# Optimization experiments

Hardware: AMD Instinct MI355X
Metric: run time of the kernel (lower is better)

## Reference

```python
import jax, jax.numpy as jnp
import numpy as np

EPS = 1e-12  # F.normalize default eps


def setup_inputs() -> dict:
    key = jax.random.key(0)
    k1, k2, k3 = jax.random.split(key, 3)
    B, C, H, W = 4, 64, 64, 64
    background = jax.random.normal(k1, (B, C, H, W), dtype=jnp.float32)
    foreground = jax.random.normal(k2, (B, C, H, W), dtype=jnp.float32)
    # binary mask, broadcast over channels
    mask = jnp.round(jax.random.uniform(k3, (B, 1, H, W), dtype=jnp.float32))
    return {"background": background, "foreground": foreground, "mask": mask}


def _l2norm(x, axis):
    # matches torch F.normalize: x / max(||x||, eps)
    n = jnp.sqrt(jnp.sum(x * x, axis=axis, keepdims=True))
    return x / jnp.maximum(n, EPS)


def reference(background, foreground, mask):
    B, C, H, W = background.shape
    bg_flat = background.reshape(B, C, H * W)   # [B, C, K]
    fg_flat = foreground.reshape(B, C, H * W)   # [B, C, Q]
    norm_bg = _l2norm(bg_flat, axis=1)
    norm_fg = _l2norm(fg_flat, axis=1)
    # cosine-similarity scores [B, K, Q]
    attention = jnp.einsum('bck,bcq->bkq', norm_bg, norm_fg)
    attention = jax.nn.softmax(attention, axis=1)  # over bg (key) axis
    attended = jnp.einsum('bck,bkq->bcq', bg_flat, attention)
    attended = attended.reshape(B, C, H, W)
    return foreground * (1.0 - mask) + attended * mask
```

## Files before the change

kernel.cpp:

```cpp
#include <hip/hip_runtime.h>
#include <math.h>

#define CC 64
#define HWN 4096
#define QB 64
#define KSPLIT 4
#define KT 32
#define NCH (HWN / KSPLIT / KT)

typedef __attribute__((ext_vector_type(8))) short bf16x8;
typedef __attribute__((ext_vector_type(4))) float f32x4;

__device__ __align__(16) unsigned short g_bgT[4][HWN][CC];
__device__ __align__(16) unsigned short g_bgN[4][CC][HWN];
__device__ __align__(16) unsigned short g_fgT[4][HWN][CC];

static __device__ __forceinline__ unsigned int f2bf(float x) {
  union { float f; unsigned int u; } v; v.f = x;
  return (v.u + 0x7fffu + ((v.u >> 16) & 1u)) >> 16;
}
static __device__ __forceinline__ unsigned int packbf(float lo, float hi) {
  return f2bf(lo) | (f2bf(hi) << 16);
}

__global__ __launch_bounds__(256) void prep_kernel(const float* __restrict__ bg,
                                                   const float* __restrict__ fg) {
  __shared__ float lds[64 * 65];
  const int bid = blockIdx.x;
  const int kt = bid & 63, b = (bid >> 6) & 3, which = bid >> 8;
  const float* src = (which ? fg : bg) + (size_t)b * CC * HWN + kt * 64;
  const int tid = threadIdx.x;

  {
    int c = tid >> 2, k0 = (tid & 3) * 16;
#pragma unroll
    for (int j4 = 0; j4 < 4; ++j4) {
      float4 v = *(const float4*)(src + (size_t)c * HWN + k0 + 4 * j4);
      lds[(k0 + 4 * j4 + 0) * 65 + c] = v.x;
      lds[(k0 + 4 * j4 + 1) * 65 + c] = v.y;
      lds[(k0 + 4 * j4 + 2) * 65 + c] = v.z;
      lds[(k0 + 4 * j4 + 3) * 65 + c] = v.w;
    }
  }
  __syncthreads();

  const int k = tid >> 2, u = tid & 3;
  float ss = 0.f;
#pragma unroll
  for (int j = 0; j < 16; ++j) {
    float v = lds[k * 65 + u * 16 + j];
    ss = fmaf(v, v, ss);
  }
  ss += __shfl_xor(ss, 1, 64);
  ss += __shfl_xor(ss, 2, 64);
  const float s = 1.0f / fmaxf(sqrtf(ss), 1e-12f);

  {
    unsigned int* gT32 = (unsigned int*)(which ? &g_fgT[0][0][0] : &g_bgT[0][0][0]);
    size_t R = (size_t)b * HWN + kt * 64 + k;
    unsigned int w8[8];
#pragma unroll
    for (int i = 0; i < 8; ++i) {
      int c2 = u * 16 + 2 * i;
      w8[i] = packbf(lds[k * 65 + c2] * s, lds[k * 65 + c2 + 1] * s);
    }
    *(uint4*)&gT32[R * 32 + u * 8]     = make_uint4(w8[0], w8[1], w8[2], w8[3]);
    *(uint4*)&gT32[R * 32 + u * 8 + 4] = make_uint4(w8[4], w8[5], w8[6], w8[7]);
  }

  if (which == 0) {
    unsigned int* gN32 = (unsigned int*)&g_bgN[0][0][0];
    int cN = tid >> 2, vN = tid & 3;
    unsigned int n8[8];
#pragma unroll
    for (int i = 0; i < 8; ++i) {
      int kk = vN * 16 + 2 * i;
      n8[i] = packbf(lds[kk * 65 + cN], lds[(kk + 1) * 65 + cN]);
    }
    size_t RN = ((size_t)b * CC + cN) * (HWN / 2) + kt * 32 + vN * 8;
    *(uint4*)&gN32[RN]     = make_uint4(n8[0], n8[1], n8[2], n8[3]);
    *(uint4*)&gN32[RN + 4] = make_uint4(n8[4], n8[5], n8[6], n8[7]);
  }
}

#define SMEM_BYTES 87040
__global__ __launch_bounds__(512, 2) void attn_kernel(const float* __restrict__ fg,
                                                      const float* __restrict__ mask,
                                                      float* __restrict__ out) {
  __shared__ __align__(16) char smem[SMEM_BYTES];
  const int b = blockIdx.y;
  const int q0 = blockIdx.x * QB;
  const int tid = threadIdx.x;
  const int lane = tid & 63;
  const int w = tid >> 6;
  const int qg = w & 1;
  const int ks = w >> 1;
  const int m16 = lane & 15;
  const int quad = lane >> 4;

  bf16x8 Bf[2][2];
  {
    int qrow = q0 + qg * 32;
#pragma unroll
    for (int qf = 0; qf < 2; ++qf)
#pragma unroll
      for (int h = 0; h < 2; ++h)
        Bf[qf][h] = *(const bf16x8*)&g_fgT[b][qrow + qf * 16 + m16][h * 32 + quad * 8];
  }

  const unsigned short* srcT[2];
  const unsigned short* srcN[2];
  int offT[2];
  int offN[2];
#pragma unroll
  for (int t = 0; t < 2; ++t) {
    int ub = (t * 2 + qg) * 64;
    int uT = ub + lane;
    int kk = uT >> 3, pos = uT & 7, j = pos ^ (kk & 7);
    srcT[t] = &g_bgT[b][ks * 1024 + kk][j * 8];
    offT[t] = ks * 8192 + ub * 16;
    int uN = ub + lane;
    int cc = uN >> 2, pos4 = uN & 3, j4 = pos4 ^ ((cc >> 1) & 3);
    srcN[t] = &g_bgN[b][cc][ks * 1024 + j4 * 8];
    offN[t] = ks * 8192 + 4096 + ub * 16;
  }

  unsigned short* P = (unsigned short*)(smem + 65536 + w * 2560);
  float* mL = (float*)(smem + 86016);

  float l_run[2] = {0.f, 0.f};
  f32x4 O[4][2];
#pragma unroll
  for (int t = 0; t < 4; ++t)
#pragma unroll
    for (int qf = 0; qf < 2; ++qf) O[t][qf] = (f32x4){0.f, 0.f, 0.f, 0.f};

  const int posN = quad ^ ((m16 >> 1) & 3);

  auto stage = [&](int bufoff) {
#pragma unroll
    for (int t = 0; t < 2; ++t) {
      __builtin_amdgcn_global_load_lds(
          (const __attribute__((address_space(1))) unsigned int*)srcT[t],
          (__attribute__((address_space(3))) unsigned int*)(smem + bufoff + offT[t]), 16, 0, 0);
      __builtin_amdgcn_global_load_lds(
          (const __attribute__((address_space(1))) unsigned int*)srcN[t],
          (__attribute__((address_space(3))) unsigned int*)(smem + bufoff + offN[t]), 16, 0, 0);
      srcT[t] += KT * CC;
      srcN[t] += KT;
    }
  };

  stage(0);
  __syncthreads();

  int bufoff = 0;
  for (int it = 0; it < NCH; ++it) {
    if (it + 1 < NCH) stage(bufoff ^ 32768);

    const char* baseT = smem + bufoff + ks * 8192;
    const char* baseN = baseT + 4096;

    f32x4 S[2][2];
#pragma unroll
    for (int i = 0; i < 2; ++i) {
      int kk = 16 * i + m16;
      bf16x8 A0 = *(const bf16x8*)(baseT + kk * 128 + ((quad) ^ (kk & 7)) * 16);
      bf16x8 A1 = *(const bf16x8*)(baseT + kk * 128 + ((4 + quad) ^ (kk & 7)) * 16);
#pragma unroll
      for (int qf = 0; qf < 2; ++qf) {
        f32x4 acc = {0.f, 0.f, 0.f, 0.f};
        acc = __builtin_amdgcn_mfma_f32_16x16x32_bf16(A0, Bf[qf][0], acc, 0, 0, 0);
        acc = __builtin_amdgcn_mfma_f32_16x16x32_bf16(A1, Bf[qf][1], acc, 0, 0, 0);
        S[qf][i] = acc;
      }
    }

#pragma unroll
    for (int qf = 0; qf < 2; ++qf) {
      float pe[2][4];
      float ps = 0.f;
#pragma unroll
      for (int i = 0; i < 2; ++i)
#pragma unroll
        for (int r = 0; r < 4; ++r) {
          pe[i][r] = __expf(S[qf][i][r] - 1.0f);
          ps += pe[i][r];
        }
      ps += __shfl_xor(ps, 16, 64);
      ps += __shfl_xor(ps, 32, 64);
      l_run[qf] += ps;
#pragma unroll
      for (int i = 0; i < 2; ++i) {
        union { float f; unsigned int u; } x0, x1, x2, x3;
        x0.f = pe[i][0]; x1.f = pe[i][1]; x2.f = pe[i][2]; x3.f = pe[i][3];
        unsigned int p01 = __builtin_amdgcn_perm(x1.u + 0x8000u, x0.u + 0x8000u, 0x07060302u);
        unsigned int p23 = __builtin_amdgcn_perm(x3.u + 0x8000u, x2.u + 0x8000u, 0x07060302u);
        *(uint2*)&P[(qf * 16 + m16) * 40 + 16 * i + quad * 4] = make_uint2(p01, p23);
      }
    }

    bf16x8 Pf0 = *(const bf16x8*)&P[m16 * 40 + quad * 8];
    bf16x8 Pf1 = *(const bf16x8*)&P[(16 + m16) * 40 + quad * 8];
#pragma unroll
    for (int t = 0; t < 4; ++t) {
      int c = 16 * t + m16;
      bf16x8 A = *(const bf16x8*)(baseN + c * 64 + posN * 16);
      O[t][0] = __builtin_amdgcn_mfma_f32_16x16x32_bf16(A, Pf0, O[t][0], 0, 0, 0);
      O[t][1] = __builtin_amdgcn_mfma_f32_16x16x32_bf16(A, Pf1, O[t][1], 0, 0, 0);
    }

    __syncthreads();
    bufoff ^= 32768;
  }

  if (quad == 0) {
    mL[w * 32 + m16] = l_run[0];
    mL[w * 32 + 16 + m16] = l_run[1];
  }
  float* mO = (float*)smem;
  const float* fgB = fg + (size_t)b * CC * HWN;
  const float* mk = mask + (size_t)b * HWN;
  float* outB = out + (size_t)b * CC * HWN;

#pragma unroll
  for (int half = 0; half < 2; ++half) {
    __syncthreads();
    if (qg == half) {
#pragma unroll
      for (int t = 0; t < 4; ++t)
#pragma unroll
        for (int qf = 0; qf < 2; ++qf)
#pragma unroll
          for (int r = 0; r < 4; ++r)
            mO[(ks * 64 + 16 * t + quad * 4 + r) * 34 + qf * 16 + m16] = O[t][qf][r];
    }
    __syncthreads();
    {
      int q = tid & 31, cb = tid >> 5;
      int qglob = q0 + half * 32 + q;
      float L = mL[(0 * 2 + half) * 32 + q] + mL[(1 * 2 + half) * 32 + q] +
                mL[(2 * 2 + half) * 32 + q] + mL[(3 * 2 + half) * 32 + q];
      float invL = 1.0f / L;
      float mv = mk[qglob];
#pragma unroll
      for (int e = 0; e < 4; ++e) {
        int c = cb * 4 + e;
        float acc = mO[(0 * 64 + c) * 34 + q] + mO[(1 * 64 + c) * 34 + q] +
                    mO[(2 * 64 + c) * 34 + q] + mO[(3 * 64 + c) * 34 + q];
        float att = acc * invL;
        float fgv = fgB[(size_t)c * HWN + qglob];
        outB[(size_t)c * HWN + qglob] = fgv + mv * (att - fgv);
      }
    }
  }
}

extern "C" void kernel_launch(void* const* d_in, const int* in_sizes, int n_in,
                              void* d_out, int out_size, void* d_ws, size_t ws_size,
                              hipStream_t stream) {
  const float* background = (const float*)d_in[0];
  const float* foreground = (const float*)d_in[1];
  const float* mask       = (const float*)d_in[2];
  float* out = (float*)d_out;
  prep_kernel<<<512, 256, 0, stream>>>(background, foreground);
  attn_kernel<<<dim3(HWN / QB, 4), 512, 0, stream>>>(foreground, mask, out);
}
```

Baseline: 101.7 us.

## Give each wave a private key slice, halve query block, drop per-iteration barriers

Halves the query tile to 32 and the block to 4 waves, one per key split. Each wave now stages and reads only its own LDS region, so the per-iteration __syncthreads is replaced by per-wave s_waitcnt vmcnt waits on the async global-to-LDS loads. MFMA sections are wrapped in s_setprio, and the epilogue becomes a single-pass reduction. The cost is twice as many blocks, each streaming the full background, so L2 traffic for the key/value tiles doubles and the foreground fragment loads are repeated per wave.

New measurement: 105.5 us. +3.7%, slower.

```diff
diff --git a/kernel.cpp b/kernel.cpp
--- a/kernel.cpp
+++ b/kernel.cpp
@@ -3,7 +3,7 @@
 
 #define CC 64
 #define HWN 4096
-#define QB 64
+#define QB 32
 #define KSPLIT 4
 #define KT 32
 #define NCH (HWN / KSPLIT / KT)
@@ -83,8 +83,10 @@
   }
 }
 
-#define SMEM_BYTES 87040
-__global__ __launch_bounds__(512, 2) void attn_kernel(const float* __restrict__ fg,
+#define P_OFF 65536
+#define ML_OFF 75776
+#define SMEM_BYTES 76288
+__global__ __launch_bounds__(256, 2) void attn_kernel(const float* __restrict__ fg,
                                                       const float* __restrict__ mask,
                                                       float* __restrict__ out) {
   __shared__ __align__(16) char smem[SMEM_BYTES];
@@ -92,41 +94,35 @@
   const int q0 = blockIdx.x * QB;
   const int tid = threadIdx.x;
   const int lane = tid & 63;
-  const int w = tid >> 6;
-  const int qg = w & 1;
-  const int ks = w >> 1;
+  const int ks = tid >> 6;
   const int m16 = lane & 15;
   const int quad = lane >> 4;
 
   bf16x8 Bf[2][2];
-  {
-    int qrow = q0 + qg * 32;
-#pragma unroll
-    for (int qf = 0; qf < 2; ++qf)
-#pragma unroll
-      for (int h = 0; h < 2; ++h)
-        Bf[qf][h] = *(const bf16x8*)&g_fgT[b][qrow + qf * 16 + m16][h * 32 + quad * 8];
-  }
-
-  const unsigned short* srcT[2];
-  const unsigned short* srcN[2];
-  int offT[2];
-  int offN[2];
-#pragma unroll
-  for (int t = 0; t < 2; ++t) {
-    int ub = (t * 2 + qg) * 64;
+#pragma unroll
+  for (int qf = 0; qf < 2; ++qf)
+#pragma unroll
+    for (int h = 0; h < 2; ++h)
+      Bf[qf][h] = *(const bf16x8*)&g_fgT[b][q0 + qf * 16 + m16][h * 32 + quad * 8];
+
+  const unsigned short* srcT[4];
+  const unsigned short* srcN[4];
+  int offT[4];
+  int offN[4];
+#pragma unroll
+  for (int t = 0; t < 4; ++t) {
+    int ub = t * 64;
     int uT = ub + lane;
     int kk = uT >> 3, pos = uT & 7, j = pos ^ (kk & 7);
     srcT[t] = &g_bgT[b][ks * 1024 + kk][j * 8];
     offT[t] = ks * 8192 + ub * 16;
-    int uN = ub + lane;
-    int cc = uN >> 2, pos4 = uN & 3, j4 = pos4 ^ ((cc >> 1) & 3);
+    int cc = uT >> 2, pos4 = uT & 3, j4 = pos4 ^ ((cc >> 1) & 3);
     srcN[t] = &g_bgN[b][cc][ks * 1024 + j4 * 8];
     offN[t] = ks * 8192 + 4096 + ub * 16;
   }
 
-  unsigned short* P = (unsigned short*)(smem + 65536 + w * 2560);
-  float* mL = (float*)(smem + 86016);
+  unsigned short* P = (unsigned short*)(smem + P_OFF + ks * 2560);
+  float* mL = (float*)(smem + ML_OFF);
 
   float l_run[2] = {0.f, 0.f};
   f32x4 O[4][2];
@@ -139,7 +135,7 @@
 
   auto stage = [&](int bufoff) {
 #pragma unroll
-    for (int t = 0; t < 2; ++t) {
+    for (int t = 0; t < 4; ++t) {
       __builtin_amdgcn_global_load_lds(
           (const __attribute__((address_space(1))) unsigned int*)srcT[t],
           (__attribute__((address_space(3))) unsigned int*)(smem + bufoff + offT[t]), 16, 0, 0);
@@ -152,16 +148,21 @@
   };
 
   stage(0);
-  __syncthreads();
-
-  int bufoff = 0;
+
+  int buf = 0;
   for (int it = 0; it < NCH; ++it) {
-    if (it + 1 < NCH) stage(bufoff ^ 32768);
-
-    const char* baseT = smem + bufoff + ks * 8192;
+    if (it + 1 < NCH) {
+      stage(buf ^ 32768);
+      asm volatile("s_waitcnt vmcnt(8)" ::: "memory");
+    } else {
+      asm volatile("s_waitcnt vmcnt(0)" ::: "memory");
+    }
+
+    const char* baseT = smem + buf + ks * 8192;
     const char* baseN = baseT + 4096;
 
     f32x4 S[2][2];
+    __builtin_amdgcn_s_setprio(1);
 #pragma unroll
     for (int i = 0; i < 2; ++i) {
       int kk = 16 * i + m16;
@@ -175,6 +176,7 @@
         S[qf][i] = acc;
       }
     }
+    __builtin_amdgcn_s_setprio(0);
 
 #pragma unroll
     for (int qf = 0; qf < 2; ++qf) {
@@ -202,6 +204,7 @@
 
     bf16x8 Pf0 = *(const bf16x8*)&P[m16 * 40 + quad * 8];
     bf16x8 Pf1 = *(const bf16x8*)&P[(16 + m16) * 40 + quad * 8];
+    __builtin_amdgcn_s_setprio(1);
 #pragma unroll
     for (int t = 0; t < 4; ++t) {
       int c = 16 * t + m16;
@@ -209,49 +212,42 @@
       O[t][0] = __builtin_amdgcn_mfma_f32_16x16x32_bf16(A, Pf0, O[t][0], 0, 0, 0);
       O[t][1] = __builtin_amdgcn_mfma_f32_16x16x32_bf16(A, Pf1, O[t][1], 0, 0, 0);
     }
-
-    __syncthreads();
-    bufoff ^= 32768;
+    __builtin_amdgcn_s_setprio(0);
+
+    buf ^= 32768;
   }
 
   if (quad == 0) {
-    mL[w * 32 + m16] = l_run[0];
-    mL[w * 32 + 16 + m16] = l_run[1];
-  }
+    mL[ks * 32 + m16] = l_run[0];
+    mL[ks * 32 + 16 + m16] = l_run[1];
+  }
+  __syncthreads();
   float* mO = (float*)smem;
-  const float* fgB = fg + (size_t)b * CC * HWN;
-  const float* mk = mask + (size_t)b * HWN;
-  float* outB = out + (size_t)b * CC * HWN;
-
-#pragma unroll
-  for (int half = 0; half < 2; ++half) {
-    __syncthreads();
-    if (qg == half) {
-#pragma unroll
-      for (int t = 0; t < 4; ++t)
-#pragma unroll
-        for (int qf = 0; qf < 2; ++qf)
-#pragma unroll
-          for (int r = 0; r < 4; ++r)
-            mO[(ks * 64 + 16 * t + quad * 4 + r) * 34 + qf * 16 + m16] = O[t][qf][r];
-    }
-    __syncthreads();
-    {
-      int q = tid & 31, cb = tid >> 5;
-      int qglob = q0 + half * 32 + q;
-      float L = mL[(0 * 2 + half) * 32 + q] + mL[(1 * 2 + half) * 32 + q] +
-                mL[(2 * 2 + half) * 32 + q] + mL[(3 * 2 + half) * 32 + q];
-      float invL = 1.0f / L;
-      float mv = mk[qglob];
-#pragma unroll
-      for (int e = 0; e < 4; ++e) {
-        int c = cb * 4 + e;
-        float acc = mO[(0 * 64 + c) * 34 + q] + mO[(1 * 64 + c) * 34 + q] +
-                    mO[(2 * 64 + c) * 34 + q] + mO[(3 * 64 + c) * 34 + q];
-        float att = acc * invL;
-        float fgv = fgB[(size_t)c * HWN + qglob];
-        outB[(size_t)c * HWN + qglob] = fgv + mv * (att - fgv);
-      }
+#pragma unroll
+  for (int t = 0; t < 4; ++t)
+#pragma unroll
+    for (int qf = 0; qf < 2; ++qf)
+#pragma unroll
+      for (int r = 0; r < 4; ++r)
+        mO[(ks * 64 + 16 * t + quad * 4 + r) * 34 + qf * 16 + m16] = O[t][qf][r];
+  __syncthreads();
+  {
+    const float* fgB = fg + (size_t)b * CC * HWN;
+    const float* mk = mask + (size_t)b * HWN;
+    float* outB = out + (size_t)b * CC * HWN;
+    int q = tid & 31, cb = tid >> 5;
+    int qglob = q0 + q;
+    float L = mL[0 * 32 + q] + mL[1 * 32 + q] + mL[2 * 32 + q] + mL[3 * 32 + q];
+    float invL = 1.0f / L;
+    float mv = mk[qglob];
+#pragma unroll
+    for (int e = 0; e < 8; ++e) {
+      int c = cb * 8 + e;
+      float acc = mO[(0 * 64 + c) * 34 + q] + mO[(1 * 64 + c) * 34 + q] +
+                  mO[(2 * 64 + c) * 34 + q] + mO[(3 * 64 + c) * 34 + q];
+      float att = acc * invL;
+      float fgv = fgB[(size_t)c * HWN + qglob];
+      outB[(size_t)c * HWN + qglob] = fgv + mv * (att - fgv);
     }
   }
 }
@@ -264,5 +260,5 @@
   const float* mask       = (const float*)d_in[2];
   float* out = (float*)d_out;
   prep_kernel<<<512, 256, 0, stream>>>(background, foreground);
-  attn_kernel<<<dim3(HWN / QB, 4), 512, 0, stream>>>(foreground, mask, out);
-}
+  attn_kernel<<<dim3(HWN / QB, 4), 256, 0, stream>>>(foreground, mask, out);
+}
```
